# Kernel tuning notes

Hardware: AMD Instinct MI355X
Metric: run time of the kernel (lower is better)

## Reference

```python
import jax, jax.numpy as jnp
import numpy as np

B, T, N, D = 2, 16, 512, 256
HID, HEADS = 256, 8
HD = HID // HEADS // 2  # 16
SCALE = HD ** -0.5
LAMBDA_INIT = 0.8 - 0.6 * float(np.exp(-0.3 * (2 - 1)))  # layer_idx = 2
LN_EPS = 1e-5


def setup_inputs() -> dict:
    key = jax.random.key(0)
    ks = jax.random.split(key, 8)
    return {
        "x": jax.random.normal(ks[0], (B, T, N, D), dtype=jnp.float32),
        "Wq": jax.random.normal(ks[1], (D, HID), dtype=jnp.float32) * (D ** -0.5),
        "Wk": jax.random.normal(ks[2], (D, HID), dtype=jnp.float32) * (D ** -0.5),
        "Wv": jax.random.normal(ks[3], (D, HID), dtype=jnp.float32) * (D ** -0.5),
        "lq1": jax.random.normal(ks[4], (HD,), dtype=jnp.float32) * 0.1,
        "lk1": jax.random.normal(ks[5], (HD,), dtype=jnp.float32) * 0.1,
        "lq2": jax.random.normal(ks[6], (HD,), dtype=jnp.float32) * 0.1,
        "lk2": jax.random.normal(ks[7], (HD,), dtype=jnp.float32) * 0.1,
        "ln_gamma": jnp.ones((2 * HD,), dtype=jnp.float32),
        "ln_beta": jnp.zeros((2 * HD,), dtype=jnp.float32),
    }


def _attn_pair(q, k, v1, v2):
    # q,k,v*: [BT, N, H, HD]; shared softmax applied to both value halves
    p = jax.nn.softmax(jnp.einsum('bnhd,bmhd->bhnm', q, k) * SCALE, axis=-1)
    o1 = jnp.einsum('bhnm,bmhd->bnhd', p, v1)
    o2 = jnp.einsum('bhnm,bmhd->bnhd', p, v2)
    return jnp.concatenate([o1, o2], axis=-1)  # [BT, N, H, 2*HD]


def reference(x, Wq, Wk, Wv, lq1, lk1, lq2, lk2, ln_gamma, ln_beta):
    b, t, n, d = x.shape
    # 1x1 Conv2d over channel dim == per-token linear projection
    q = jnp.einsum('btnd,dh->btnh', x, Wq).reshape(b * t, n, HEADS, 2 * HD)
    k = jnp.einsum('btnd,dh->btnh', x, Wk).reshape(b * t, n, HEADS, 2 * HD)
    v = jnp.einsum('btnd,dh->btnh', x, Wv).reshape(b * t, n, HEADS, 2 * HD)
    q1, q2 = jnp.split(q, 2, axis=-1)
    k1, k2 = jnp.split(k, 2, axis=-1)
    v1, v2 = jnp.split(v, 2, axis=-1)
    attn1 = _attn_pair(q1, k1, v1, v2)
    attn2 = _attn_pair(q2, k2, v1, v2)
    lam = jnp.exp(jnp.sum(lq1 * lk1)) - jnp.exp(jnp.sum(lq2 * lk2)) + LAMBDA_INIT
    y = attn1 - lam * attn2  # [BT, N, H, 2*HD]
    mu = jnp.mean(y, axis=-1, keepdims=True)
    var = jnp.mean(jnp.square(y - mu), axis=-1, keepdims=True)
    y = (y - mu) * jax.lax.rsqrt(var + LN_EPS) * ln_gamma + ln_beta
    y = y * (1.0 - LAMBDA_INIT)
    return y.reshape(b, t, n, HEADS * 2 * HD)
```

## Files before the change

### kernel.cpp

```cpp
#include <hip/hip_runtime.h>
#include <cmath>

typedef unsigned short u16;
typedef unsigned int   u32;
typedef __attribute__((ext_vector_type(8)))  short short8;
typedef __attribute__((ext_vector_type(4)))  float f32x4;
typedef __attribute__((ext_vector_type(16))) float f32x16;

constexpr int BT    = 32;
constexpr int NTOK  = 512;
constexpr int DIM   = 256;
constexpr int HID   = 256;
constexpr int M_ROWS = BT * NTOK;
constexpr int HM     = M_ROWS * 32;
constexpr size_t TENS = (size_t)M_ROWS * HID;
constexpr float LAMBDA_INIT  = 0.35550906759096927f;
constexpr float ONE_MINUS_LI = 0.6444909324090307f;
constexpr float LN_EPS = 1e-5f;
constexpr float QSCALE = 0.36067376022224085f;

#define MFMA16(a, b, c) __builtin_amdgcn_mfma_f32_16x16x32_bf16((a), (b), (c), 0, 0, 0)
#define MFMA32(a, b, c) __builtin_amdgcn_mfma_f32_32x32x16_bf16((a), (b), (c), 0, 0, 0)

__device__ __forceinline__ u16 f2bf(float f) {
    u32 u = __float_as_uint(f);
    return (u16)((u + 0x7FFFu + ((u >> 16) & 1u)) >> 16);
}

__device__ __forceinline__ float fexp2(float x) {
#if defined(__has_builtin) && __has_builtin(__builtin_amdgcn_exp2f)
    return __builtin_amdgcn_exp2f(x);
#else
    return exp2f(x);
#endif
}

__device__ __forceinline__ u32 pack_trunc(float a, float b) {
    return __builtin_amdgcn_perm(__float_as_uint(b), __float_as_uint(a), 0x07060302u);
}

__device__ __forceinline__ short8 ldb64x2(const u16* p) {
    uint2 a = *(const uint2*)p;
    uint2 b = *(const uint2*)(p + 4);
    union { u32 u[4]; short8 s; } x;
    x.u[0] = a.x; x.u[1] = a.y; x.u[2] = b.x; x.u[3] = b.y;
    return x.s;
}

__global__ __launch_bounds__(256) void prep_w(const float* __restrict__ Wq,
                                              const float* __restrict__ Wk,
                                              const float* __restrict__ Wv,
                                              u16* __restrict__ Wt) {
    const float* W = (blockIdx.z == 0) ? Wq : (blockIdx.z == 1) ? Wk : Wv;
    u16* dst = Wt + (size_t)blockIdx.z * 65536;
    __shared__ float T[64][65];
    const int k0 = blockIdx.x * 64, n0 = blockIdx.y * 64;
    const int tr = threadIdx.x >> 4;
    const int tc = threadIdx.x & 15;
    #pragma unroll
    for (int i = 0; i < 4; ++i) {
        int row = tr + i * 16;
        float4 v = *(const float4*)&W[(size_t)(k0 + row) * HID + n0 + tc * 4];
        T[row][tc * 4 + 0] = v.x; T[row][tc * 4 + 1] = v.y;
        T[row][tc * 4 + 2] = v.z; T[row][tc * 4 + 3] = v.w;
    }
    __syncthreads();
    #pragma unroll
    for (int i = 0; i < 4; ++i) {
        int n = tr + i * 16;
        int k4 = tc * 4;
        uint2 pk;
        pk.x = (u32)f2bf(T[k4 + 0][n]) | ((u32)f2bf(T[k4 + 1][n]) << 16);
        pk.y = (u32)f2bf(T[k4 + 2][n]) | ((u32)f2bf(T[k4 + 3][n]) << 16);
        *(uint2*)&dst[(size_t)(n0 + n) * DIM + k0 + k4] = pk;
    }
}

__global__ __launch_bounds__(256, 4) void proj_kernel(
    const float* __restrict__ x, const u16* __restrict__ Wt,
    u16* __restrict__ Qh, u16* __restrict__ Kh, u16* __restrict__ Vh)
{
    __shared__ u16 As[64 * 72];
    __shared__ u16 Bs[3][64 * 72];

    const int tid  = threadIdx.x;
    const int n0   = blockIdx.x * 64;
    const int m0   = blockIdx.y * 64;
    const int lane = tid & 63;
    const int wv   = tid >> 6;
    const int q16  = lane & 15;
    const int quad = lane >> 4;
    const int mw   = (wv >> 1) * 32;
    const int nw   = (wv & 1) * 32;

    const int sr = tid >> 2;
    const int sc = (tid & 3) * 16;

    f32x4 acc[3][4];
    #pragma unroll
    for (int z = 0; z < 3; ++z)
        #pragma unroll
        for (int t = 0; t < 4; ++t)
            acc[z][t] = (f32x4){0.f, 0.f, 0.f, 0.f};

    float4 ga[4];
    uint4  gb[3][2];
    {
        const float4* xs = (const float4*)&x[(size_t)(m0 + sr) * DIM + sc];
        ga[0] = xs[0]; ga[1] = xs[1]; ga[2] = xs[2]; ga[3] = xs[3];
        #pragma unroll
        for (int z = 0; z < 3; ++z) {
            const uint4* ws4 = (const uint4*)&Wt[(size_t)z * 65536 + (size_t)(n0 + sr) * DIM + sc];
            gb[z][0] = ws4[0]; gb[z][1] = ws4[1];
        }
    }

    for (int it = 0; it < 4; ++it) {
        {
            uint4 o0, o1;
            o0.x = (u32)f2bf(ga[0].x) | ((u32)f2bf(ga[0].y) << 16);
            o0.y = (u32)f2bf(ga[0].z) | ((u32)f2bf(ga[0].w) << 16);
            o0.z = (u32)f2bf(ga[1].x) | ((u32)f2bf(ga[1].y) << 16);
            o0.w = (u32)f2bf(ga[1].z) | ((u32)f2bf(ga[1].w) << 16);
            o1.x = (u32)f2bf(ga[2].x) | ((u32)f2bf(ga[2].y) << 16);
            o1.y = (u32)f2bf(ga[2].z) | ((u32)f2bf(ga[2].w) << 16);
            o1.z = (u32)f2bf(ga[3].x) | ((u32)f2bf(ga[3].y) << 16);
            o1.w = (u32)f2bf(ga[3].z) | ((u32)f2bf(ga[3].w) << 16);
            *(uint4*)&As[sr * 72 + sc]     = o0;
            *(uint4*)&As[sr * 72 + sc + 8] = o1;
            #pragma unroll
            for (int z = 0; z < 3; ++z) {
                *(uint4*)&Bs[z][sr * 72 + sc]     = gb[z][0];
                *(uint4*)&Bs[z][sr * 72 + sc + 8] = gb[z][1];
            }
        }
        __syncthreads();

        if (it < 3) {
            const int kk = (it + 1) * 64;
            const float4* xs = (const float4*)&x[(size_t)(m0 + sr) * DIM + kk + sc];
            ga[0] = xs[0]; ga[1] = xs[1]; ga[2] = xs[2]; ga[3] = xs[3];
            #pragma unroll
            for (int z = 0; z < 3; ++z) {
                const uint4* ws4 = (const uint4*)&Wt[(size_t)z * 65536 + (size_t)(n0 + sr) * DIM + kk + sc];
                gb[z][0] = ws4[0]; gb[z][1] = ws4[1];
            }
        }

        #pragma unroll
        for (int kc = 0; kc < 2; ++kc) {
            short8 a0 = *(const short8*)&As[(mw +      q16) * 72 + kc * 32 + quad * 8];
            short8 a1 = *(const short8*)&As[(mw + 16 + q16) * 72 + kc * 32 + quad * 8];
            #pragma unroll
            for (int z = 0; z < 3; ++z) {
                short8 b0 = *(const short8*)&Bs[z][(nw +      q16) * 72 + kc * 32 + quad * 8];
                short8 b1 = *(const short8*)&Bs[z][(nw + 16 + q16) * 72 + kc * 32 + quad * 8];
                acc[z][0] = MFMA16(b0, a0, acc[z][0]);
                acc[z][1] = MFMA16(b1, a0, acc[z][1]);
                acc[z][2] = MFMA16(b0, a1, acc[z][2]);
                acc[z][3] = MFMA16(b1, a1, acc[z][3]);
            }
        }
        __syncthreads();
    }

    const int hcol = (n0 + nw) >> 5;
    #pragma unroll
    for (int z = 0; z < 3; ++z) {
        u16* C = (z == 0) ? Qh : (z == 1) ? Kh : Vh;
        u16* base = C + (size_t)hcol * HM;
        const float s = (z == 0) ? QSCALE : 1.0f;
        #pragma unroll
        for (int t = 0; t < 4; ++t) {
            const int m  = m0 + mw + ((t >> 1) << 4) + q16;
            const int c0 = ((t & 1) << 4) + quad * 4;
            uint2 w;
            w.x = (u32)f2bf(acc[z][t][0] * s) | ((u32)f2bf(acc[z][t][1] * s) << 16);
            w.y = (u32)f2bf(acc[z][t][2] * s) | ((u32)f2bf(acc[z][t][3] * s) << 16);
            *(uint2*)&base[(size_t)m * 32 + c0] = w;
        }
    }
}

__global__ __launch_bounds__(256, 3) void attn_kernel(
    const u16* __restrict__ Qh, const u16* __restrict__ Kh, const u16* __restrict__ Vh,
    const float* __restrict__ lq1, const float* __restrict__ lk1,
    const float* __restrict__ lq2, const float* __restrict__ lk2,
    const float* __restrict__ gamma, const float* __restrict__ beta,
    float* __restrict__ out)
{
    __shared__ u16 Ks[256 * 36];
    __shared__ u16 Vts[32 * 264];
    __shared__ u16 Pb[4][2][32 * 36];

    const int qh  = blockIdx.x;
    const int h   = blockIdx.y;
    const int bt  = blockIdx.z;
    const int tid = threadIdx.x;
    const int lane = tid & 63;
    const int wv   = tid >> 6;
    const int l31  = lane & 31;
    const int hi   = lane >> 5;

    float sa = 0.f, sb = 0.f;
    #pragma unroll
    for (int d = 0; d < 16; ++d) { sa += lq1[d] * lk1[d]; sb += lq2[d] * lk2[d]; }
    const float lam = __expf(sa) - __expf(sb) + LAMBDA_INIT;

    const int qbase = bt * NTOK + qh * 128 + wv * 32;
    const u16* qrowp = Qh + (size_t)h * HM + (size_t)(qbase + l31) * 32 + hi * 8;
    const short8 B1 = *(const short8*)qrowp;
    const short8 B2 = *(const short8*)(qrowp + 16);

    const f32x16 z16 = {0.f,0.f,0.f,0.f,0.f,0.f,0.f,0.f,0.f,0.f,0.f,0.f,0.f,0.f,0.f,0.f};
    f32x16 O1 = z16, O2 = z16;
    float l1 = 0.f, l2 = 0.f;
    u16* P1 = &Pb[wv][0][0];
    u16* P2 = &Pb[wv][1][0];

    for (int chunk = 0; chunk < 2; ++chunk) {
        if (chunk) __syncthreads();
        {
            const uint4* src = (const uint4*)(Kh + (size_t)h * HM +
                                (size_t)(bt * NTOK + chunk * 256 + tid) * 32);
            union { uint4 q[4]; uint2 d[8]; } kb;
            kb.q[0] = src[0]; kb.q[1] = src[1]; kb.q[2] = src[2]; kb.q[3] = src[3];
            uint2* dst = (uint2*)&Ks[tid * 36];
            #pragma unroll
            for (int i = 0; i < 8; ++i) dst[i] = kb.d[i];
        }
        if (tid < 128) {
            const int j0 = tid * 2;
            const u16* v0 = Vh + (size_t)h * HM + (size_t)(bt * NTOK + chunk * 256 + j0) * 32;
            union U { uint4 q[4]; u32 w[16]; } ra, rb;
            #pragma unroll
            for (int i = 0; i < 4; ++i) {
                ra.q[i] = ((const uint4*)v0)[i];
                rb.q[i] = ((const uint4*)(v0 + 32))[i];
            }
            #pragma unroll
            for (int w = 0; w < 16; ++w) {
                u32 lo  = __builtin_amdgcn_perm(rb.w[w], ra.w[w], 0x05040100u);
                u32 hi2 = __builtin_amdgcn_perm(rb.w[w], ra.w[w], 0x07060302u);
                *(u32*)&Vts[(2 * w)     * 264 + j0] = lo;
                *(u32*)&Vts[(2 * w + 1) * 264 + j0] = hi2;
            }
        }
        __syncthreads();

        for (int kc = 0; kc < 8; ++kc) {
            const u16* krow = &Ks[(kc * 32 + l31) * 36];
            const short8 A1 = ldb64x2(krow + hi * 8);
            const short8 A2 = ldb64x2(krow + 16 + hi * 8);
            const u16* vrow = &Vts[l31 * 264 + kc * 32 + hi * 8];
            const short8 Vt0 = *(const short8*)vrow;
            const short8 Vt1 = *(const short8*)(vrow + 16);

            f32x16 S1 = MFMA32(A1, B1, z16);
            f32x16 S2 = MFMA32(A2, B2, z16);
            #pragma unroll
            for (int rg = 0; rg < 4; ++rg) {
                float e0 = fexp2(S1[4 * rg + 0]);
                float e1 = fexp2(S1[4 * rg + 1]);
                float e2 = fexp2(S1[4 * rg + 2]);
                float e3 = fexp2(S1[4 * rg + 3]);
                l1 += (e0 + e1) + (e2 + e3);
                uint2 w; w.x = pack_trunc(e0, e1); w.y = pack_trunc(e2, e3);
                *(uint2*)&P1[l31 * 36 + rg * 8 + hi * 4] = w;
            }
            #pragma unroll
            for (int rg = 0; rg < 4; ++rg) {
                float e0 = fexp2(S2[4 * rg + 0]);
                float e1 = fexp2(S2[4 * rg + 1]);
                float e2 = fexp2(S2[4 * rg + 2]);
                float e3 = fexp2(S2[4 * rg + 3]);
                l2 += (e0 + e1) + (e2 + e3);
                uint2 w; w.x = pack_trunc(e0, e1); w.y = pack_trunc(e2, e3);
                *(uint2*)&P2[l31 * 36 + rg * 8 + hi * 4] = w;
            }
            {
                const short8 Pa0 = ldb64x2(&P1[l31 * 36 + hi * 8]);
                const short8 Pa1 = ldb64x2(&P1[l31 * 36 + 16 + hi * 8]);
                const short8 Pb0 = ldb64x2(&P2[l31 * 36 + hi * 8]);
                const short8 Pb1 = ldb64x2(&P2[l31 * 36 + 16 + hi * 8]);
                O1 = MFMA32(Pa0, Vt0, O1);
                O1 = MFMA32(Pa1, Vt1, O1);
                O2 = MFMA32(Pb0, Vt0, O2);
                O2 = MFMA32(Pb1, Vt1, O2);
            }
        }
    }

    l1 += __shfl_xor(l1, 32);
    l2 += __shfl_xor(l2, 32);
    const float i1base = 1.0f / l1;
    const float i2base = 1.0f / l2;
    const float g  = gamma[l31];
    const float bc = beta[l31];

    #pragma unroll
    for (int r = 0; r < 16; ++r) {
        const int qloc = (r & 3) + 8 * (r >> 2) + 4 * hi;
        const float i1 = __shfl(i1base, qloc);
        const float i2 = __shfl(i2base, qloc);
        float y = O1[r] * i1 - lam * (O2[r] * i2);

        float s  = y;
        float s2 = y * y;
        #pragma unroll
        for (int off = 1; off < 32; off <<= 1) {
            s  += __shfl_xor(s,  off);
            s2 += __shfl_xor(s2, off);
        }
        const float mu   = s * (1.0f / 32.0f);
        const float var  = s2 * (1.0f / 32.0f) - mu * mu;
        const float rstd = rsqrtf(var + LN_EPS);

        const int row = qbase + qloc;
        out[(size_t)row * HID + h * 32 + l31] = ((y - mu) * rstd * g + bc) * ONE_MINUS_LI;
    }
}

extern "C" void kernel_launch(void* const* d_in, const int* in_sizes, int n_in,
                              void* d_out, int out_size, void* d_ws, size_t ws_size,
                              hipStream_t stream) {
    const float* x   = (const float*)d_in[0];
    const float* Wq  = (const float*)d_in[1];
    const float* Wk  = (const float*)d_in[2];
    const float* Wv  = (const float*)d_in[3];
    const float* lq1 = (const float*)d_in[4];
    const float* lk1 = (const float*)d_in[5];
    const float* lq2 = (const float*)d_in[6];
    const float* lk2 = (const float*)d_in[7];
    const float* gam = (const float*)d_in[8];
    const float* bet = (const float*)d_in[9];
    float* out = (float*)d_out;

    u16* ws = (u16*)d_ws;
    u16* Wt = ws;
    u16* Qh = Wt + 3 * 65536;
    u16* Kh = Qh + TENS;
    u16* Vh = Kh + TENS;

    hipLaunchKernelGGL(prep_w, dim3(4, 4, 3), dim3(256), 0, stream, Wq, Wk, Wv, Wt);
    hipLaunchKernelGGL(proj_kernel, dim3(HID / 64, M_ROWS / 64), dim3(256), 0, stream,
                       x, Wt, Qh, Kh, Vh);
    hipLaunchKernelGGL(attn_kernel, dim3(4, 8, 32), dim3(256), 0, stream,
                       Qh, Kh, Vh, lq1, lk1, lq2, lk2, gam, bet, out);
}
```

Before: 159.8 us.

## Replace LDS P round-trip with cross-lane shuffles and restage K/QKV stores

The attention kernel no longer writes softmax probabilities to shared memory and reads them back. It rebuilds the MFMA A-operand fragment by exchanging packed bf16 pairs between lane halves with shfl_xor. K is staged in shared memory in a fragment-ordered layout so each lane does one 16-byte read instead of two 8-byte reads, and the P buffer is removed, which allows the occupancy hint to rise from 3 to 4. The projection epilogue now stages tiles in shared memory to issue coalesced 16-byte global stores. Risks: the shuffle/select code adds VALU and cross-lane traffic, and the higher occupancy target may cause register spills.

```diff
diff --git a/kernel.cpp b/kernel.cpp
--- a/kernel.cpp
+++ b/kernel.cpp
@@ -37,14 +37,6 @@
 
 __device__ __forceinline__ u32 pack_trunc(float a, float b) {
     return __builtin_amdgcn_perm(__float_as_uint(b), __float_as_uint(a), 0x07060302u);
-}
-
-__device__ __forceinline__ short8 ldb64x2(const u16* p) {
-    uint2 a = *(const uint2*)p;
-    uint2 b = *(const uint2*)(p + 4);
-    union { u32 u[4]; short8 s; } x;
-    x.u[0] = a.x; x.u[1] = a.y; x.u[2] = b.x; x.u[3] = b.y;
-    return x.s;
 }
 
 __global__ __launch_bounds__(256) void prep_w(const float* __restrict__ Wq,
@@ -164,34 +156,38 @@
         __syncthreads();
     }
 
+    u16* Ep = &As[wv * 1152];
     const int hcol = (n0 + nw) >> 5;
     #pragma unroll
     for (int z = 0; z < 3; ++z) {
-        u16* C = (z == 0) ? Qh : (z == 1) ? Kh : Vh;
-        u16* base = C + (size_t)hcol * HM;
         const float s = (z == 0) ? QSCALE : 1.0f;
         #pragma unroll
         for (int t = 0; t < 4; ++t) {
-            const int m  = m0 + mw + ((t >> 1) << 4) + q16;
-            const int c0 = ((t & 1) << 4) + quad * 4;
             uint2 w;
             w.x = (u32)f2bf(acc[z][t][0] * s) | ((u32)f2bf(acc[z][t][1] * s) << 16);
             w.y = (u32)f2bf(acc[z][t][2] * s) | ((u32)f2bf(acc[z][t][3] * s) << 16);
-            *(uint2*)&base[(size_t)m * 32 + c0] = w;
-        }
-    }
-}
-
-__global__ __launch_bounds__(256, 3) void attn_kernel(
+            *(uint2*)&Ep[((t >> 1) * 16 + q16) * 36 + (t & 1) * 16 + quad * 4] = w;
+        }
+        u16* C = (z == 0) ? Qh : (z == 1) ? Kh : Vh;
+        u16* gbase = C + (size_t)hcol * HM + (size_t)(m0 + mw) * 32;
+        #pragma unroll
+        for (int i = 0; i < 2; ++i) {
+            const int lrow = i * 16 + (lane >> 2);
+            uint4 v = *(const uint4*)&Ep[lrow * 36 + (lane & 3) * 8];
+            *(uint4*)&gbase[(size_t)lrow * 32 + (lane & 3) * 8] = v;
+        }
+    }
+}
+
+__global__ __launch_bounds__(256, 4) void attn_kernel(
     const u16* __restrict__ Qh, const u16* __restrict__ Kh, const u16* __restrict__ Vh,
     const float* __restrict__ lq1, const float* __restrict__ lk1,
     const float* __restrict__ lq2, const float* __restrict__ lk2,
     const float* __restrict__ gamma, const float* __restrict__ beta,
     float* __restrict__ out)
 {
-    __shared__ u16 Ks[256 * 36];
+    __shared__ u16 Ks[256 * 64];
     __shared__ u16 Vts[32 * 264];
-    __shared__ u16 Pb[4][2][32 * 36];
 
     const int qh  = blockIdx.x;
     const int h   = blockIdx.y;
@@ -208,30 +204,30 @@
     const float lam = __expf(sa) - __expf(sb) + LAMBDA_INIT;
 
     const int qbase = bt * NTOK + qh * 128 + wv * 32;
-    const u16* qrowp = Qh + (size_t)h * HM + (size_t)(qbase + l31) * 32 + hi * 8;
+    const size_t hbase = (size_t)h * HM;
+    const u16* qrowp = Qh + hbase + (size_t)(qbase + l31) * 32 + hi * 8;
     const short8 B1 = *(const short8*)qrowp;
     const short8 B2 = *(const short8*)(qrowp + 16);
 
     const f32x16 z16 = {0.f,0.f,0.f,0.f,0.f,0.f,0.f,0.f,0.f,0.f,0.f,0.f,0.f,0.f,0.f,0.f};
     f32x16 O1 = z16, O2 = z16;
     float l1 = 0.f, l2 = 0.f;
-    u16* P1 = &Pb[wv][0][0];
-    u16* P2 = &Pb[wv][1][0];
 
     for (int chunk = 0; chunk < 2; ++chunk) {
         if (chunk) __syncthreads();
         {
-            const uint4* src = (const uint4*)(Kh + (size_t)h * HM +
+            const uint4* src = (const uint4*)(Kh + hbase +
                                 (size_t)(bt * NTOK + chunk * 256 + tid) * 32);
-            union { uint4 q[4]; uint2 d[8]; } kb;
-            kb.q[0] = src[0]; kb.q[1] = src[1]; kb.q[2] = src[2]; kb.q[3] = src[3];
-            uint2* dst = (uint2*)&Ks[tid * 36];
-            #pragma unroll
-            for (int i = 0; i < 8; ++i) dst[i] = kb.d[i];
+            uint4 r0 = src[0], r1 = src[1], r2 = src[2], r3 = src[3];
+            u16* d0 = &Ks[((tid >> 5) * 128 + (tid & 31)) * 8];
+            *(uint4*)(d0 + 0 * 256) = r0;
+            *(uint4*)(d0 + 1 * 256) = r1;
+            *(uint4*)(d0 + 2 * 256) = r2;
+            *(uint4*)(d0 + 3 * 256) = r3;
         }
         if (tid < 128) {
             const int j0 = tid * 2;
-            const u16* v0 = Vh + (size_t)h * HM + (size_t)(bt * NTOK + chunk * 256 + j0) * 32;
+            const u16* v0 = Vh + hbase + (size_t)(bt * NTOK + chunk * 256 + j0) * 32;
             union U { uint4 q[4]; u32 w[16]; } ra, rb;
             #pragma unroll
             for (int i = 0; i < 4; ++i) {
@@ -249,44 +245,52 @@
         __syncthreads();
 
         for (int kc = 0; kc < 8; ++kc) {
-            const u16* krow = &Ks[(kc * 32 + l31) * 36];
-            const short8 A1 = ldb64x2(krow + hi * 8);
-            const short8 A2 = ldb64x2(krow + 16 + hi * 8);
+            const int tb = kc * 1024;
+            const short8 A1 = *(const short8*)&Ks[tb + lane * 8];
+            const short8 A2 = *(const short8*)&Ks[tb + 512 + lane * 8];
             const u16* vrow = &Vts[l31 * 264 + kc * 32 + hi * 8];
             const short8 Vt0 = *(const short8*)vrow;
             const short8 Vt1 = *(const short8*)(vrow + 16);
 
-            f32x16 S1 = MFMA32(A1, B1, z16);
-            f32x16 S2 = MFMA32(A2, B2, z16);
-            #pragma unroll
-            for (int rg = 0; rg < 4; ++rg) {
-                float e0 = fexp2(S1[4 * rg + 0]);
-                float e1 = fexp2(S1[4 * rg + 1]);
-                float e2 = fexp2(S1[4 * rg + 2]);
-                float e3 = fexp2(S1[4 * rg + 3]);
-                l1 += (e0 + e1) + (e2 + e3);
-                uint2 w; w.x = pack_trunc(e0, e1); w.y = pack_trunc(e2, e3);
-                *(uint2*)&P1[l31 * 36 + rg * 8 + hi * 4] = w;
-            }
-            #pragma unroll
-            for (int rg = 0; rg < 4; ++rg) {
-                float e0 = fexp2(S2[4 * rg + 0]);
-                float e1 = fexp2(S2[4 * rg + 1]);
-                float e2 = fexp2(S2[4 * rg + 2]);
-                float e3 = fexp2(S2[4 * rg + 3]);
-                l2 += (e0 + e1) + (e2 + e3);
-                uint2 w; w.x = pack_trunc(e0, e1); w.y = pack_trunc(e2, e3);
-                *(uint2*)&P2[l31 * 36 + rg * 8 + hi * 4] = w;
-            }
-            {
-                const short8 Pa0 = ldb64x2(&P1[l31 * 36 + hi * 8]);
-                const short8 Pa1 = ldb64x2(&P1[l31 * 36 + 16 + hi * 8]);
-                const short8 Pb0 = ldb64x2(&P2[l31 * 36 + hi * 8]);
-                const short8 Pb1 = ldb64x2(&P2[l31 * 36 + 16 + hi * 8]);
-                O1 = MFMA32(Pa0, Vt0, O1);
-                O1 = MFMA32(Pa1, Vt1, O1);
-                O2 = MFMA32(Pb0, Vt0, O2);
-                O2 = MFMA32(Pb1, Vt1, O2);
+            const f32x16 S1 = MFMA32(A1, B1, z16);
+            const f32x16 S2 = MFMA32(A2, B2, z16);
+
+            #pragma unroll
+            for (int ch = 0; ch < 2; ++ch) {
+                const f32x16& S = ch ? S2 : S1;
+                float e[16];
+                #pragma unroll
+                for (int j = 0; j < 16; ++j) e[j] = fexp2(S[j]);
+                float ls = ((e[0]+e[1])+(e[2]+e[3])) + ((e[4]+e[5])+(e[6]+e[7]))
+                         + ((e[8]+e[9])+(e[10]+e[11])) + ((e[12]+e[13])+(e[14]+e[15]));
+                if (ch) l2 += ls; else l1 += ls;
+                u32 dw[8];
+                #pragma unroll
+                for (int i = 0; i < 8; ++i) dw[i] = pack_trunc(e[2*i], e[2*i+1]);
+                u32 s0 = hi ? dw[0] : dw[2];
+                u32 s1 = hi ? dw[1] : dw[3];
+                u32 s2 = hi ? dw[4] : dw[6];
+                u32 s3 = hi ? dw[5] : dw[7];
+                u32 r0 = (u32)__shfl_xor((int)s0, 32);
+                u32 r1 = (u32)__shfl_xor((int)s1, 32);
+                u32 r2 = (u32)__shfl_xor((int)s2, 32);
+                u32 r3 = (u32)__shfl_xor((int)s3, 32);
+                union { u32 u[4]; short8 s; } f1, f2;
+                f1.u[0] = hi ? r0    : dw[0];
+                f1.u[1] = hi ? r1    : dw[1];
+                f1.u[2] = hi ? dw[2] : r0;
+                f1.u[3] = hi ? dw[3] : r1;
+                f2.u[0] = hi ? r2    : dw[4];
+                f2.u[1] = hi ? r3    : dw[5];
+                f2.u[2] = hi ? dw[6] : r2;
+                f2.u[3] = hi ? dw[7] : r3;
+                if (ch) {
+                    O2 = MFMA32(f1.s, Vt0, O2);
+                    O2 = MFMA32(f2.s, Vt1, O2);
+                } else {
+                    O1 = MFMA32(f1.s, Vt0, O1);
+                    O1 = MFMA32(f2.s, Vt1, O1);
+                }
             }
         }
     }
```

Result: slower. 180.7 us (+13.1%).
